# Optimization experiments

Measured on AMD Instinct MI355X. Metric: run time of the kernel, lower is better.

The kernel has to match this reference:

```python
import jax, jax.numpy as jnp
import numpy as np

N_PATHS = 200000
PATH_LEN = 8
N_LINKS = 20000
MAX_PL = 100  # max paths crossing a link
DIM = 16
ITERS = 8
# min-max normalization constants: (min, scale) as in set_min_max_scores
MM_TRAFFIC = (0.0, 1e-4)
MM_PACKETS = (0.0, 1e-2)
MM_PKTSIZE = (0.0, 1e-3)
MM_CAP = (0.0, 1e-1)


def _gru(x, h, k, rk, b):
    # Keras GRUCell, reset_after=True. b: [2, 3*units] (input bias, recurrent bias)
    mx = x @ k + b[0]
    mi = h @ rk + b[1]
    xz, xr, xh = jnp.split(mx, 3, axis=-1)
    rz, rr, rh = jnp.split(mi, 3, axis=-1)
    z = jax.nn.sigmoid(xz + rz)
    r = jax.nn.sigmoid(xr + rr)
    hh = jnp.tanh(xh + r * rh)
    return z * h + (1.0 - z) * hh


def setup_inputs() -> dict:
    key = jax.random.key(0)
    ks = jax.random.split(key, 24)
    f32 = jnp.float32
    inp = {}
    inp['flow_traffic'] = jax.random.uniform(ks[0], (N_PATHS, 1), f32, 100.0, 10000.0)
    inp['flow_packets'] = jax.random.uniform(ks[1], (N_PATHS, 1), f32, 1.0, 100.0)
    inp['flow_packet_size'] = jax.random.uniform(ks[2], (N_PATHS, 1), f32, 100.0, 1500.0)
    inp['flow_type'] = jax.random.uniform(ks[3], (N_PATHS, 2), f32)
    inp['link_capacity'] = jax.random.uniform(ks[4], (N_LINKS, 1), f32, 10.0, 100.0)
    inp['link_to_path'] = jax.random.randint(ks[5], (N_PATHS, PATH_LEN), 0, N_LINKS, jnp.int32)
    p_idx = jax.random.randint(ks[6], (N_LINKS, MAX_PL), 0, N_PATHS, jnp.int32)
    s_idx = jax.random.randint(ks[7], (N_LINKS, MAX_PL), 0, PATH_LEN + 1, jnp.int32)
    inp['path_to_link'] = jnp.stack([p_idx, s_idx], axis=-1)

    def dense(k, i, o):
        return jax.random.normal(k, (i, o), f32) * (1.0 / np.sqrt(i))

    inp['fe_w1'] = dense(ks[8], 5, DIM);   inp['fe_b1'] = jnp.zeros((DIM,), f32)
    inp['fe_w2'] = dense(ks[9], DIM, DIM); inp['fe_b2'] = jnp.zeros((DIM,), f32)
    inp['le_w1'] = dense(ks[10], 2, DIM);  inp['le_b1'] = jnp.zeros((DIM,), f32)
    inp['le_w2'] = dense(ks[11], DIM, DIM); inp['le_b2'] = jnp.zeros((DIM,), f32)
    inp['pgru_k'] = dense(ks[12], DIM, 3 * DIM)
    inp['pgru_rk'] = dense(ks[13], DIM, 3 * DIM)
    inp['pgru_b'] = jnp.zeros((2, 3 * DIM), f32)
    inp['lgru_k'] = dense(ks[14], DIM, 3 * DIM)
    inp['lgru_rk'] = dense(ks[15], DIM, 3 * DIM)
    inp['lgru_b'] = jnp.zeros((2, 3 * DIM), f32)
    inp['ro_w1'] = dense(ks[16], DIM, DIM // 2); inp['ro_b1'] = jnp.zeros((DIM // 2,), f32)
    inp['ro_w2'] = dense(ks[17], DIM // 2, DIM // 4); inp['ro_b2'] = jnp.zeros((DIM // 4,), f32)
    inp['ro_w3'] = dense(ks[18], DIM // 4, 1); inp['ro_b3'] = jnp.zeros((1,), f32)
    return inp


def reference(flow_traffic, flow_packets, flow_packet_size, flow_type, link_capacity,
              link_to_path, path_to_link,
              fe_w1, fe_b1, fe_w2, fe_b2, le_w1, le_b1, le_w2, le_b2,
              pgru_k, pgru_rk, pgru_b, lgru_k, lgru_rk, lgru_b,
              ro_w1, ro_b1, ro_w2, ro_b2, ro_w3, ro_b3):
    relu = jax.nn.relu
    # load per link: sum traffic of crossing paths / capacity
    load = jnp.sum(flow_traffic[path_to_link[:, :, 0]], axis=1) / (link_capacity * 1e9)  # [L,1]

    flow_feats = jnp.concatenate([
        (flow_traffic - MM_TRAFFIC[0]) * MM_TRAFFIC[1],
        (flow_packets - MM_PACKETS[0]) * MM_PACKETS[1],
        (flow_packet_size - MM_PKTSIZE[0]) * MM_PKTSIZE[1],
        flow_type], axis=1)  # [P,5]
    path_state = relu(relu(flow_feats @ fe_w1 + fe_b1) @ fe_w2 + fe_b2)  # [P,16]

    link_feats = jnp.concatenate([(link_capacity - MM_CAP[0]) * MM_CAP[1], load], axis=1)  # [L,2]
    link_state = relu(relu(link_feats @ le_w1 + le_b1) @ le_w2 + le_b2)  # [L,16]

    for _ in range(ITERS):
        link_gather = link_state[link_to_path]  # [P, path_len, 16]
        prev = path_state

        def step(h, x):
            h2 = _gru(x, h, pgru_k, pgru_rk, pgru_b)
            return h2, h2

        path_state, seq = jax.lax.scan(step, prev, jnp.swapaxes(link_gather, 0, 1))
        seq = jnp.swapaxes(seq, 0, 1)  # [P, path_len, 16]
        path_state_sequence = jnp.concatenate([prev[:, None, :], seq], axis=1)  # [P, path_len+1, 16]
        # gather_nd: (path_idx, seq_pos) pairs per link
        path_gather = path_state_sequence[path_to_link[:, :, 0], path_to_link[:, :, 1]]  # [L, MAX_PL, 16]
        path_sum = jnp.sum(path_gather, axis=1)  # [L,16]
        link_state = _gru(path_sum, link_state, lgru_k, lgru_rk, lgru_b)

    h1 = relu(path_state_sequence[:, 1:] @ ro_w1 + ro_b1)
    h2 = relu(h1 @ ro_w2 + ro_b2)
    occupancy = jax.nn.softplus(h2 @ ro_w3 + ro_b3)  # [P, path_len, 1]
    capacity_gather = link_capacity[link_to_path]  # [P, path_len, 1]
    delay = jnp.sum(occupancy / capacity_gather, axis=1)  # [P,1]
    return delay
```

## Files before the change

### kernel.cpp

```cpp
#include <hip/hip_runtime.h>
#include <hip/hip_bf16.h>
#include <math.h>

#define N_PATHS  200000
#define PATH_LEN 8
#define N_LINKS  20000
#define MAX_PL   100
#define DIM      16
#define ITERS    8

typedef __attribute__((ext_vector_type(8))) short bf16x8;
typedef __attribute__((ext_vector_type(4))) float f32x4;

#define SEQ_BYTES 64000000ull
#define LS_BYTES  1280000ull
#define LXK_BYTES 1920000ull
#define P2L_BYTES 8000000ull

__device__ __forceinline__ float fast_sigmoid(float x) {
    return __builtin_amdgcn_rcpf(1.0f + __expf(-x));
}
__device__ __forceinline__ float fast_tanh(float x) {
    float ax = fabsf(x);
    float t  = __expf(-2.0f * ax);
    float r  = (1.0f - t) * __builtin_amdgcn_rcpf(1.0f + t);
    return copysignf(r, x);
}
__device__ __forceinline__ float softplusf_(float x) {
    return fmaxf(x, 0.0f) + log1pf(expf(-fabsf(x)));
}
__device__ __forceinline__ float bflo(unsigned int u) {
    union { unsigned int i; float f; } c; c.i = u << 16; return c.f;
}
__device__ __forceinline__ float bfhi(unsigned int u) {
    union { unsigned int i; float f; } c; c.i = u & 0xffff0000u; return c.f;
}
__device__ __forceinline__ unsigned int pk_bf16(float lo, float hi) {
    unsigned int r;
    asm("v_cvt_pk_bf16_f32 %0, %1, %2" : "=v"(r) : "v"(lo), "v"(hi));
    return r;
}

union U8 { unsigned int u[4]; bf16x8 v; };

__global__ __launch_bounds__(256) void k_pack(const int* __restrict__ p2l,
                                              unsigned int* __restrict__ outE,
                                              unsigned int* __restrict__ outO)
{
    int i = blockIdx.x * 256 + threadIdx.x;
    if (i < N_LINKS * MAX_PL) {
        unsigned int pi = (unsigned int)p2l[2 * i];
        unsigned int si = (unsigned int)p2l[2 * i + 1];
        unsigned int sE = (si == 0) ? 8u : ((si == 8) ? 9u : si);
        unsigned int sO = (si == 0) ? 9u : ((si == 8) ? 8u : si);
        outE[i] = (sE << 18) | pi;
        outO[i] = (sO << 18) | pi;
    }
}

__global__ __launch_bounds__(64) void k_init_links(
    const float* __restrict__ traffic, const float* __restrict__ cap,
    const int* __restrict__ p2l,
    const float* __restrict__ le_w1, const float* __restrict__ le_b1,
    const float* __restrict__ le_w2, const float* __restrict__ le_b2,
    const float* __restrict__ pk, const float* __restrict__ pb,
    float* __restrict__ ls, unsigned short* __restrict__ lxk)
{
    int l = blockIdx.x;
    int lane = threadIdx.x;
    float s = 0.0f;
    for (int j = lane; j < MAX_PL; j += 64) {
        int p = p2l[(size_t)(l * MAX_PL + j) * 2 + 0];
        s += traffic[p];
    }
    #pragma unroll
    for (int off = 32; off > 0; off >>= 1) s += __shfl_xor(s, off);

    float c = cap[l];
    float f0 = c * 0.1f;
    float f1 = s / (c * 1e9f);

    float h1[DIM];
    #pragma unroll
    for (int d = 0; d < DIM; d++)
        h1[d] = fmaxf(f0 * le_w1[d] + f1 * le_w1[DIM + d] + le_b1[d], 0.0f);

    float h2[DIM];
    #pragma unroll
    for (int d = 0; d < DIM; d++) {
        float a = le_b2[d];
        #pragma unroll
        for (int k = 0; k < DIM; k++) a = fmaf(h1[k], le_w2[k * DIM + d], a);
        h2[d] = fmaxf(a, 0.0f);
    }
    if (lane < DIM) ls[(size_t)l * DIM + lane] = h2[lane];
    if (lane < 48) {
        float a = pb[lane];
        #pragma unroll
        for (int k = 0; k < DIM; k++) a = fmaf(h2[k], pk[k * 48 + lane], a);
        lxk[(size_t)l * 48 + lane] = (unsigned short)(pk_bf16(a, a) & 0xffffu);
    }
}

__global__ __launch_bounds__(256) void k_init_paths(
    const float* __restrict__ traffic, const float* __restrict__ packets,
    const float* __restrict__ pktsize, const float* __restrict__ ftype,
    const float* __restrict__ fe_w1, const float* __restrict__ fe_b1,
    const float* __restrict__ fe_w2, const float* __restrict__ fe_b2,
    unsigned short* __restrict__ seq)
{
    int p = blockIdx.x * blockDim.x + threadIdx.x;
    if (p >= N_PATHS) return;
    float f[5];
    f[0] = traffic[p] * 0.0001f;
    f[1] = packets[p] * 0.01f;
    f[2] = pktsize[p] * 0.001f;
    f[3] = ftype[p * 2 + 0];
    f[4] = ftype[p * 2 + 1];

    float h1[DIM];
    #pragma unroll
    for (int d = 0; d < DIM; d++) {
        float a = fe_b1[d];
        #pragma unroll
        for (int k = 0; k < 5; k++) a = fmaf(f[k], fe_w1[k * DIM + d], a);
        h1[d] = fmaxf(a, 0.0f);
    }
    float h2[DIM];
    #pragma unroll
    for (int d = 0; d < DIM; d++) {
        float a = fe_b2[d];
        #pragma unroll
        for (int k = 0; k < DIM; k++) a = fmaf(h1[k], fe_w2[k * DIM + d], a);
        h2[d] = fmaxf(a, 0.0f);
    }
    unsigned int pkd[8];
    #pragma unroll
    for (int q = 0; q < 8; q++) pkd[q] = pk_bf16(h2[2 * q], h2[2 * q + 1]);
    uint4* out = (uint4*)(seq + ((size_t)8 * N_PATHS + p) * DIM);
    out[0] = make_uint4(pkd[0], pkd[1], pkd[2], pkd[3]);
    out[1] = make_uint4(pkd[4], pkd[5], pkd[6], pkd[7]);
}

__global__ __launch_bounds__(256) void k_paths(
    const int* __restrict__ l2p, const unsigned short* __restrict__ lxk,
    const float* __restrict__ rk, const float* __restrict__ b,
    unsigned short* __restrict__ seq, int ps, int cs)
{
    int l = threadIdx.x & 63;
    int wave = (blockIdx.x * 256 + threadIdx.x) >> 6;
    if (wave >= N_PATHS / 32) return;
    int pr = l & 15;
    int g  = l >> 4;
    int kq = g * 4;
    int pA = wave * 32 + pr;
    int pB = pA + 16;

    U8 Az, Ar, Ah;
    {
        #pragma unroll
        for (int i = 0; i < 2; i++) {
            float wz0 = rk[(kq + 2 * i) * 48 + pr] * 0.5f;
            float wz1 = rk[(kq + 2 * i + 1) * 48 + pr] * 0.5f;
            float wr0 = rk[(kq + 2 * i) * 48 + 16 + pr] * 0.5f;
            float wr1 = rk[(kq + 2 * i + 1) * 48 + 16 + pr] * 0.5f;
            float wh0 = rk[(kq + 2 * i) * 48 + 32 + pr] * 0.5f;
            float wh1 = rk[(kq + 2 * i + 1) * 48 + 32 + pr] * 0.5f;
            Az.u[i] = pk_bf16(wz0, wz1); Az.u[i + 2] = Az.u[i];
            Ar.u[i] = pk_bf16(wr0, wr1); Ar.u[i + 2] = Ar.u[i];
            Ah.u[i] = pk_bf16(wh0, wh1); Ah.u[i + 2] = Ah.u[i];
        }
    }
    f32x4 Cz, Cr, Ch;
    #pragma unroll
    for (int r = 0; r < 4; r++) {
        Cz[r] = b[48 + kq + r];
        Cr[r] = b[48 + 16 + kq + r];
        Ch[r] = b[48 + 32 + kq + r];
    }

    int2 iA = *(const int2*)(l2p + (size_t)pA * 8 + 2 * g);
    int2 iB = *(const int2*)(l2p + (size_t)pB * 8 + 2 * g);

    uint2 uzA[8], urA[8], uhA[8];
    uint2 uzB[8], urB[8], uhB[8];

#define PREF(t) { \
    int liA = __shfl(((t) & 1) ? iA.y : iA.x, pr + 16 * ((t) >> 1)); \
    const unsigned short* xa = lxk + (size_t)liA * 48 + kq; \
    uzA[t] = *(const uint2*)(xa); urA[t] = *(const uint2*)(xa + 16); uhA[t] = *(const uint2*)(xa + 32); \
    int liB = __shfl(((t) & 1) ? iB.y : iB.x, pr + 16 * ((t) >> 1)); \
    const unsigned short* xb = lxk + (size_t)liB * 48 + kq; \
    uzB[t] = *(const uint2*)(xb); urB[t] = *(const uint2*)(xb + 16); uhB[t] = *(const uint2*)(xb + 32); }

    PREF(0) PREF(1) PREF(2) PREF(3)

    float hA0, hA1, hA2, hA3, hB0, hB1, hB2, hB3;
    U8 BA, BB;
    {
        uint2 hp = *(const uint2*)(seq + ((size_t)ps * N_PATHS + pA) * DIM + kq);
        hA0 = bflo(hp.x); hA1 = bfhi(hp.x); hA2 = bflo(hp.y); hA3 = bfhi(hp.y);
        BA.u[0] = hp.x; BA.u[1] = hp.y; BA.u[2] = hp.x; BA.u[3] = hp.y;
        uint2 hq = *(const uint2*)(seq + ((size_t)ps * N_PATHS + pB) * DIM + kq);
        hB0 = bflo(hq.x); hB1 = bfhi(hq.x); hB2 = bflo(hq.y); hB3 = bfhi(hq.y);
        BB.u[0] = hq.x; BB.u[1] = hq.y; BB.u[2] = hq.x; BB.u[3] = hq.y;
    }

#define TCORE(t, os, uzX, urX, uhX, BX, h0X, h1X, h2X, h3X, pX) { \
    uint2 uz = uzX[t], ur = urX[t], uh = uhX[t]; \
    f32x4 az = __builtin_amdgcn_mfma_f32_16x16x32_bf16(Az.v, BX.v, Cz, 0, 0, 0); \
    f32x4 ar = __builtin_amdgcn_mfma_f32_16x16x32_bf16(Ar.v, BX.v, Cr, 0, 0, 0); \
    f32x4 ah = __builtin_amdgcn_mfma_f32_16x16x32_bf16(Ah.v, BX.v, Ch, 0, 0, 0); \
    float z0 = fast_sigmoid(bflo(uz.x) + az[0]), z1 = fast_sigmoid(bfhi(uz.x) + az[1]); \
    float z2 = fast_sigmoid(bflo(uz.y) + az[2]), z3 = fast_sigmoid(bfhi(uz.y) + az[3]); \
    float r0 = fast_sigmoid(bflo(ur.x) + ar[0]), r1 = fast_sigmoid(bfhi(ur.x) + ar[1]); \
    float r2 = fast_sigmoid(bflo(ur.y) + ar[2]), r3 = fast_sigmoid(bfhi(ur.y) + ar[3]); \
    float q0 = fast_tanh(bflo(uh.x) + r0 * ah[0]), q1 = fast_tanh(bfhi(uh.x) + r1 * ah[1]); \
    float q2 = fast_tanh(bflo(uh.y) + r2 * ah[2]), q3 = fast_tanh(bfhi(uh.y) + r3 * ah[3]); \
    h0X = z0 * h0X + (1.0f - z0) * q0; \
    h1X = z1 * h1X + (1.0f - z1) * q1; \
    h2X = z2 * h2X + (1.0f - z2) * q2; \
    h3X = z3 * h3X + (1.0f - z3) * q3; \
    unsigned int p01 = pk_bf16(h0X, h1X), p23 = pk_bf16(h2X, h3X); \
    *(uint2*)(seq + ((size_t)(os) * N_PATHS + pX) * DIM + kq) = make_uint2(p01, p23); \
    BX.u[0] = p01; BX.u[1] = p23; BX.u[2] = p01; BX.u[3] = p23; }

#define STEP(t, os) \
    TCORE(t, os, uzA, urA, uhA, BA, hA0, hA1, hA2, hA3, pA) \
    TCORE(t, os, uzB, urB, uhB, BB, hB0, hB1, hB2, hB3, pB)

    PREF(4) STEP(0, 1)
    PREF(5) STEP(1, 2)
    PREF(6) STEP(2, 3)
    PREF(7) STEP(3, 4)
    STEP(4, 5)
    STEP(5, 6)
    STEP(6, 7)
    STEP(7, cs)
#undef PREF
#undef TCORE
#undef STEP
}

__global__ __launch_bounds__(256) void k_links(
    const unsigned int* __restrict__ p2lp, const unsigned short* __restrict__ seq,
    const float* __restrict__ lk, const float* __restrict__ lrk,
    const float* __restrict__ lb,
    const float* __restrict__ pk, const float* __restrict__ pb,
    float* ls, unsigned short* __restrict__ lxk)
{
    int lane = threadIdx.x & 63;
    int l = blockIdx.x * 4 + (threadIdx.x >> 6);
    size_t base = (size_t)l * MAX_PL;
    int half = lane & 1;
    int r0 = lane >> 1;

    unsigned int e0 = p2lp[base + r0];
    unsigned int e1 = p2lp[base + r0 + 32];
    unsigned int e2 = p2lp[base + r0 + 64];

    const unsigned short* sh = seq + half * 8;
    unsigned int pi, si;
    pi = e0 & 0x3FFFFu; si = e0 >> 18;
    uint4 a0 = *(const uint4*)(sh + ((size_t)si * N_PATHS + pi) * DIM);
    pi = e1 & 0x3FFFFu; si = e1 >> 18;
    uint4 a1 = *(const uint4*)(sh + ((size_t)si * N_PATHS + pi) * DIM);
    pi = e2 & 0x3FFFFu; si = e2 >> 18;
    uint4 a2 = *(const uint4*)(sh + ((size_t)si * N_PATHS + pi) * DIM);

    float acc[8];
    #pragma unroll
    for (int i = 0; i < 8; i++) acc[i] = 0.0f;
    unsigned int selLo = 0x00003F80u;
    unsigned int selHi = 0x3F800000u;

#define DOTU(u, i0) \
    asm("v_dot2_f32_bf16 %0, %1, %2, %0" : "+v"(acc[i0]) : "v"(u), "v"(selLo)); \
    asm("v_dot2_f32_bf16 %0, %1, %2, %0" : "+v"(acc[i0 + 1]) : "v"(u), "v"(selHi));
#define DOT8(a) DOTU(a.x, 0) DOTU(a.y, 2) DOTU(a.z, 4) DOTU(a.w, 6)

    DOT8(a0) DOT8(a1) DOT8(a2)
    if (r0 < 4) {
        unsigned int e3 = p2lp[base + r0 + 96];
        pi = e3 & 0x3FFFFu; si = e3 >> 18;
        uint4 a3 = *(const uint4*)(sh + ((size_t)si * N_PATHS + pi) * DIM);
        DOT8(a3)
    }
#undef DOTU
#undef DOT8

    float v4[4];
    {
        int sel = (lane & 2) ? 4 : 0;
        #pragma unroll
        for (int i = 0; i < 4; i++)
            v4[i] = acc[sel + i] + __shfl_xor(acc[(4 - sel) + i], 2);
    }
    float v2[2];
    {
        int sel = (lane & 4) ? 2 : 0;
        #pragma unroll
        for (int i = 0; i < 2; i++)
            v2[i] = v4[sel + i] + __shfl_xor(v4[(2 - sel) + i], 4);
    }
    float s;
    {
        int sel = (lane & 8) ? 1 : 0;
        s = v2[sel] + __shfl_xor(v2[1 - sel], 8);
    }
    s += __shfl_xor(s, 16);
    s += __shfl_xor(s, 32);

    float accf[16];
    #pragma unroll
    for (int k = 0; k < 16; k++) {
        int src = ((k >> 3) & 1) | (((k >> 2) & 1) << 1) | (((k >> 1) & 1) << 2) | ((k & 1) << 3);
        accf[k] = __shfl(s, src);
    }

    float h[DIM];
    #pragma unroll
    for (int d = 0; d < DIM; d++) h[d] = ls[(size_t)l * DIM + d];

    int j = (lane < 48) ? lane : 0;
    float mx = lb[j];
    float mi = lb[48 + j];
    #pragma unroll
    for (int k = 0; k < DIM; k++) {
        mx = fmaf(accf[k], lk[k * 48 + j], mx);
        mi = fmaf(h[k],   lrk[k * 48 + j], mi);
    }

    int d = lane & 15;
    float xz = __shfl(mx, d),      rz = __shfl(mi, d);
    float xr = __shfl(mx, d + 16), rr = __shfl(mi, d + 16);
    float xh = __shfl(mx, d + 32), rh = __shfl(mi, d + 32);
    float z  = fast_sigmoid(xz + rz);
    float r  = fast_sigmoid(xr + rr);
    float hh = fast_tanh(xh + r * rh);
    float hn = z * h[d] + (1.0f - z) * hh;

    if (lane < DIM) ls[(size_t)l * DIM + lane] = hn;

    float hf[DIM];
    #pragma unroll
    for (int k = 0; k < DIM; k++) hf[k] = __shfl(hn, k);
    if (lane < 48) {
        float a = pb[lane];
        #pragma unroll
        for (int k = 0; k < DIM; k++) a = fmaf(hf[k], pk[k * 48 + lane], a);
        lxk[(size_t)l * 48 + lane] = (unsigned short)(pk_bf16(a, a) & 0xffffu);
    }
}

__global__ __launch_bounds__(256) void k_readout(
    const unsigned short* __restrict__ seq, const int* __restrict__ l2p,
    const float* __restrict__ cap,
    const float* __restrict__ w1, const float* __restrict__ b1,
    const float* __restrict__ w2, const float* __restrict__ b2,
    const float* __restrict__ w3, const float* __restrict__ b3,
    float* __restrict__ out)
{
    int p = blockIdx.x * blockDim.x + threadIdx.x;
    if (p >= N_PATHS) return;
    float delay = 0.0f;
    for (int t = 1; t <= PATH_LEN; t++) {
        const uint4* gp = (const uint4*)(seq + ((size_t)t * N_PATHS + p) * DIM);
        uint4 a = gp[0], c = gp[1];
        float h[DIM];
        h[0]  = bflo(a.x); h[1]  = bfhi(a.x); h[2]  = bflo(a.y); h[3]  = bfhi(a.y);
        h[4]  = bflo(a.z); h[5]  = bfhi(a.z); h[6]  = bflo(a.w); h[7]  = bfhi(a.w);
        h[8]  = bflo(c.x); h[9]  = bfhi(c.x); h[10] = bflo(c.y); h[11] = bfhi(c.y);
        h[12] = bflo(c.z); h[13] = bfhi(c.z); h[14] = bflo(c.w); h[15] = bfhi(c.w);

        float h1[8];
        #pragma unroll
        for (int jj = 0; jj < 8; jj++) {
            float a1 = b1[jj];
            #pragma unroll
            for (int k = 0; k < DIM; k++) a1 = fmaf(h[k], w1[k * 8 + jj], a1);
            h1[jj] = fmaxf(a1, 0.0f);
        }
        float h2[4];
        #pragma unroll
        for (int jj = 0; jj < 4; jj++) {
            float a2 = b2[jj];
            #pragma unroll
            for (int k = 0; k < 8; k++) a2 = fmaf(h1[k], w2[k * 4 + jj], a2);
            h2[jj] = fmaxf(a2, 0.0f);
        }
        float o = b3[0];
        #pragma unroll
        for (int k = 0; k < 4; k++) o = fmaf(h2[k], w3[k], o);
        o = softplusf_(o);

        float cp = cap[l2p[(size_t)p * PATH_LEN + (t - 1)]];
        delay += o / cp;
    }
    out[p] = delay;
}

extern "C" void kernel_launch(void* const* d_in, const int* in_sizes, int n_in,
                              void* d_out, int out_size, void* d_ws, size_t ws_size,
                              hipStream_t stream)
{
    const float* flow_traffic = (const float*)d_in[0];
    const float* flow_packets = (const float*)d_in[1];
    const float* flow_pktsize = (const float*)d_in[2];
    const float* flow_type    = (const float*)d_in[3];
    const float* link_cap     = (const float*)d_in[4];
    const int*   l2p          = (const int*)d_in[5];
    const int*   p2l          = (const int*)d_in[6];
    const float* fe_w1 = (const float*)d_in[7];
    const float* fe_b1 = (const float*)d_in[8];
    const float* fe_w2 = (const float*)d_in[9];
    const float* fe_b2 = (const float*)d_in[10];
    const float* le_w1 = (const float*)d_in[11];
    const float* le_b1 = (const float*)d_in[12];
    const float* le_w2 = (const float*)d_in[13];
    const float* le_b2 = (const float*)d_in[14];
    const float* pgru_k  = (const float*)d_in[15];
    const float* pgru_rk = (const float*)d_in[16];
    const float* pgru_b  = (const float*)d_in[17];
    const float* lgru_k  = (const float*)d_in[18];
    const float* lgru_rk = (const float*)d_in[19];
    const float* lgru_b  = (const float*)d_in[20];
    const float* ro_w1 = (const float*)d_in[21];
    const float* ro_b1 = (const float*)d_in[22];
    const float* ro_w2 = (const float*)d_in[23];
    const float* ro_b2 = (const float*)d_in[24];
    const float* ro_w3 = (const float*)d_in[25];
    const float* ro_b3 = (const float*)d_in[26];
    float* out = (float*)d_out;

    char* ws = (char*)d_ws;
    unsigned short* seq   = (unsigned short*)ws;
    float*          ls    = (float*)(ws + SEQ_BYTES);
    unsigned short* lxk   = (unsigned short*)(ws + SEQ_BYTES + LS_BYTES);
    unsigned int*   p2lpE = (unsigned int*)(ws + SEQ_BYTES + LS_BYTES + LXK_BYTES);
    unsigned int*   p2lpO = (unsigned int*)(ws + SEQ_BYTES + LS_BYTES + LXK_BYTES + P2L_BYTES);

    k_pack<<<(N_LINKS * MAX_PL + 255) / 256, 256, 0, stream>>>(p2l, p2lpE, p2lpO);
    k_init_links<<<N_LINKS, 64, 0, stream>>>(flow_traffic, link_cap, p2l,
        le_w1, le_b1, le_w2, le_b2, pgru_k, pgru_b, ls, lxk);
    k_init_paths<<<(N_PATHS + 255) / 256, 256, 0, stream>>>(flow_traffic,
        flow_packets, flow_pktsize, flow_type, fe_w1, fe_b1, fe_w2, fe_b2, seq);

    int nPathBlocks = (N_PATHS / 32 + 3) / 4;
    for (int it = 0; it < ITERS; ++it) {
        int ps = (it & 1) ? 9 : 8;
        int cs = (it & 1) ? 8 : 9;
        k_paths<<<nPathBlocks, 256, 0, stream>>>(l2p, lxk, pgru_rk, pgru_b,
            seq, ps, cs);
        if (it != ITERS - 1)
            k_links<<<N_LINKS / 4, 256, 0, stream>>>((it & 1) ? p2lpO : p2lpE,
                seq, lgru_k, lgru_rk, lgru_b, pgru_k, pgru_b, ls, lxk);
    }

    k_readout<<<(N_PATHS + 255) / 256, 256, 0, stream>>>(seq, l2p, link_cap,
        ro_w1, ro_b1, ro_w2, ro_b2, ro_w3, ro_b3, out);
}
```

Before: 638.3 us.

## Restructure path GRU kernel to one path group per wave with fp32 link projections

The path GRU kernel now gives each wave 16 paths instead of 32, which doubles the number of waves. It drops the interleaved A/B streams and, with launch bounds, asks for four blocks per CU. The precomputed link input projections (lxk) are now stored in fp32 rather than bf16, so the bf16-to-fp32 unpacking goes away at the cost of twice the gather bytes. Gate math is rewritten with packed v_pk_* f32 ops and exp2-based sigmoid and tanh, and address arithmetic uses 32-bit byte offsets. Together these aim to raise occupancy and latency hiding and to cut VALU work, but they add memory traffic on the link gathers.

```diff
diff --git a/kernel.cpp b/kernel.cpp
--- a/kernel.cpp
+++ b/kernel.cpp
@@ -11,11 +11,13 @@
 
 typedef __attribute__((ext_vector_type(8))) short bf16x8;
 typedef __attribute__((ext_vector_type(4))) float f32x4;
+typedef __attribute__((ext_vector_type(2))) float f32x2;
 
 #define SEQ_BYTES 64000000ull
 #define LS_BYTES  1280000ull
-#define LXK_BYTES 1920000ull
+#define LXK_BYTES 3840000ull
 #define P2L_BYTES 8000000ull
+#define SLOT_BYTES 6400000u
 
 __device__ __forceinline__ float fast_sigmoid(float x) {
     return __builtin_amdgcn_rcpf(1.0f + __expf(-x));
@@ -39,6 +41,32 @@
     unsigned int r;
     asm("v_cvt_pk_bf16_f32 %0, %1, %2" : "=v"(r) : "v"(lo), "v"(hi));
     return r;
+}
+
+__device__ __forceinline__ f32x2 pk_add2(f32x2 a, f32x2 b) {
+    f32x2 d; asm("v_pk_add_f32 %0, %1, %2" : "=v"(d) : "v"(a), "v"(b)); return d;
+}
+__device__ __forceinline__ f32x2 pk_mul2(f32x2 a, f32x2 b) {
+    f32x2 d; asm("v_pk_mul_f32 %0, %1, %2" : "=v"(d) : "v"(a), "v"(b)); return d;
+}
+__device__ __forceinline__ f32x2 pk_fma2(f32x2 a, f32x2 b, f32x2 c) {
+    f32x2 d; asm("v_pk_fma_f32 %0, %1, %2, %3" : "=v"(d) : "v"(a), "v"(b), "v"(c)); return d;
+}
+__device__ __forceinline__ f32x2 mk2(float a, float b) { f32x2 r; r.x = a; r.y = b; return r; }
+
+__device__ __forceinline__ f32x2 sig2(f32x2 x) {
+    f32x2 t = pk_mul2(x, mk2(-1.44269504f, -1.44269504f));
+    f32x2 e; e.x = __builtin_amdgcn_exp2f(t.x); e.y = __builtin_amdgcn_exp2f(t.y);
+    f32x2 d = pk_add2(e, mk2(1.0f, 1.0f));
+    f32x2 r; r.x = __builtin_amdgcn_rcpf(d.x); r.y = __builtin_amdgcn_rcpf(d.y);
+    return r;
+}
+__device__ __forceinline__ f32x2 tanh2(f32x2 x) {
+    f32x2 t = pk_mul2(x, mk2(2.88539008f, 2.88539008f));
+    f32x2 e; e.x = __builtin_amdgcn_exp2f(t.x); e.y = __builtin_amdgcn_exp2f(t.y);
+    f32x2 d = pk_add2(e, mk2(1.0f, 1.0f));
+    f32x2 r; r.x = __builtin_amdgcn_rcpf(d.x); r.y = __builtin_amdgcn_rcpf(d.y);
+    return pk_fma2(r, mk2(-2.0f, -2.0f), mk2(1.0f, 1.0f));
 }
 
 union U8 { unsigned int u[4]; bf16x8 v; };
@@ -64,7 +92,7 @@
     const float* __restrict__ le_w1, const float* __restrict__ le_b1,
     const float* __restrict__ le_w2, const float* __restrict__ le_b2,
     const float* __restrict__ pk, const float* __restrict__ pb,
-    float* __restrict__ ls, unsigned short* __restrict__ lxk)
+    float* __restrict__ ls, float* __restrict__ lxk)
 {
     int l = blockIdx.x;
     int lane = threadIdx.x;
@@ -98,7 +126,7 @@
         float a = pb[lane];
         #pragma unroll
         for (int k = 0; k < DIM; k++) a = fmaf(h2[k], pk[k * 48 + lane], a);
-        lxk[(size_t)l * 48 + lane] = (unsigned short)(pk_bf16(a, a) & 0xffffu);
+        lxk[(size_t)l * 48 + lane] = a;
     }
 }
 
@@ -142,19 +170,17 @@
     out[1] = make_uint4(pkd[4], pkd[5], pkd[6], pkd[7]);
 }
 
-__global__ __launch_bounds__(256) void k_paths(
-    const int* __restrict__ l2p, const unsigned short* __restrict__ lxk,
+__global__ __launch_bounds__(256, 4) void k_paths(
+    const int* __restrict__ l2p, const float* __restrict__ lxk,
     const float* __restrict__ rk, const float* __restrict__ b,
     unsigned short* __restrict__ seq, int ps, int cs)
 {
     int l = threadIdx.x & 63;
     int wave = (blockIdx.x * 256 + threadIdx.x) >> 6;
-    if (wave >= N_PATHS / 32) return;
     int pr = l & 15;
     int g  = l >> 4;
     int kq = g * 4;
-    int pA = wave * 32 + pr;
-    int pB = pA + 16;
+    int p  = wave * 16 + pr;
 
     U8 Az, Ar, Ah;
     {
@@ -179,67 +205,66 @@
         Ch[r] = b[48 + 32 + kq + r];
     }
 
-    int2 iA = *(const int2*)(l2p + (size_t)pA * 8 + 2 * g);
-    int2 iB = *(const int2*)(l2p + (size_t)pB * 8 + 2 * g);
-
-    uint2 uzA[8], urA[8], uhA[8];
-    uint2 uzB[8], urB[8], uhB[8];
-
+    int4 ia = *(const int4*)(l2p + (size_t)p * 8);
+    int4 ib = *(const int4*)(l2p + (size_t)p * 8 + 4);
+#define IDX(t) ((t) == 0 ? ia.x : (t) == 1 ? ia.y : (t) == 2 ? ia.z : (t) == 3 ? ia.w : \
+                (t) == 4 ? ib.x : (t) == 5 ? ib.y : (t) == 6 ? ib.z : ib.w)
+
+    const char* lxkc = (const char*)lxk;
+    char* seqc = (char*)seq;
+    unsigned gsh = (unsigned)(g * 16);
+    unsigned sbase = (unsigned)p * 32u + (unsigned)(g * 8);
+    unsigned csoff = (unsigned)cs * SLOT_BYTES + sbase;
+
+    float4 pz[8], prr[8], ph[8];
 #define PREF(t) { \
-    int liA = __shfl(((t) & 1) ? iA.y : iA.x, pr + 16 * ((t) >> 1)); \
-    const unsigned short* xa = lxk + (size_t)liA * 48 + kq; \
-    uzA[t] = *(const uint2*)(xa); urA[t] = *(const uint2*)(xa + 16); uhA[t] = *(const uint2*)(xa + 32); \
-    int liB = __shfl(((t) & 1) ? iB.y : iB.x, pr + 16 * ((t) >> 1)); \
-    const unsigned short* xb = lxk + (size_t)liB * 48 + kq; \
-    uzB[t] = *(const uint2*)(xb); urB[t] = *(const uint2*)(xb + 16); uhB[t] = *(const uint2*)(xb + 32); }
+    unsigned off = (unsigned)IDX(t) * 192u + gsh; \
+    const char* xp = lxkc + off; \
+    pz[t]  = *(const float4*)(xp); \
+    prr[t] = *(const float4*)(xp + 64); \
+    ph[t]  = *(const float4*)(xp + 128); }
 
     PREF(0) PREF(1) PREF(2) PREF(3)
 
-    float hA0, hA1, hA2, hA3, hB0, hB1, hB2, hB3;
-    U8 BA, BB;
+    f32x2 hA, hB;
+    U8 B;
     {
-        uint2 hp = *(const uint2*)(seq + ((size_t)ps * N_PATHS + pA) * DIM + kq);
-        hA0 = bflo(hp.x); hA1 = bfhi(hp.x); hA2 = bflo(hp.y); hA3 = bfhi(hp.y);
-        BA.u[0] = hp.x; BA.u[1] = hp.y; BA.u[2] = hp.x; BA.u[3] = hp.y;
-        uint2 hq = *(const uint2*)(seq + ((size_t)ps * N_PATHS + pB) * DIM + kq);
-        hB0 = bflo(hq.x); hB1 = bfhi(hq.x); hB2 = bflo(hq.y); hB3 = bfhi(hq.y);
-        BB.u[0] = hq.x; BB.u[1] = hq.y; BB.u[2] = hq.x; BB.u[3] = hq.y;
-    }
-
-#define TCORE(t, os, uzX, urX, uhX, BX, h0X, h1X, h2X, h3X, pX) { \
-    uint2 uz = uzX[t], ur = urX[t], uh = uhX[t]; \
-    f32x4 az = __builtin_amdgcn_mfma_f32_16x16x32_bf16(Az.v, BX.v, Cz, 0, 0, 0); \
-    f32x4 ar = __builtin_amdgcn_mfma_f32_16x16x32_bf16(Ar.v, BX.v, Cr, 0, 0, 0); \
-    f32x4 ah = __builtin_amdgcn_mfma_f32_16x16x32_bf16(Ah.v, BX.v, Ch, 0, 0, 0); \
-    float z0 = fast_sigmoid(bflo(uz.x) + az[0]), z1 = fast_sigmoid(bfhi(uz.x) + az[1]); \
-    float z2 = fast_sigmoid(bflo(uz.y) + az[2]), z3 = fast_sigmoid(bfhi(uz.y) + az[3]); \
-    float r0 = fast_sigmoid(bflo(ur.x) + ar[0]), r1 = fast_sigmoid(bfhi(ur.x) + ar[1]); \
-    float r2 = fast_sigmoid(bflo(ur.y) + ar[2]), r3 = fast_sigmoid(bfhi(ur.y) + ar[3]); \
-    float q0 = fast_tanh(bflo(uh.x) + r0 * ah[0]), q1 = fast_tanh(bfhi(uh.x) + r1 * ah[1]); \
-    float q2 = fast_tanh(bflo(uh.y) + r2 * ah[2]), q3 = fast_tanh(bfhi(uh.y) + r3 * ah[3]); \
-    h0X = z0 * h0X + (1.0f - z0) * q0; \
-    h1X = z1 * h1X + (1.0f - z1) * q1; \
-    h2X = z2 * h2X + (1.0f - z2) * q2; \
-    h3X = z3 * h3X + (1.0f - z3) * q3; \
-    unsigned int p01 = pk_bf16(h0X, h1X), p23 = pk_bf16(h2X, h3X); \
-    *(uint2*)(seq + ((size_t)(os) * N_PATHS + pX) * DIM + kq) = make_uint2(p01, p23); \
-    BX.u[0] = p01; BX.u[1] = p23; BX.u[2] = p01; BX.u[3] = p23; }
-
-#define STEP(t, os) \
-    TCORE(t, os, uzA, urA, uhA, BA, hA0, hA1, hA2, hA3, pA) \
-    TCORE(t, os, uzB, urB, uhB, BB, hB0, hB1, hB2, hB3, pB)
-
-    PREF(4) STEP(0, 1)
-    PREF(5) STEP(1, 2)
-    PREF(6) STEP(2, 3)
-    PREF(7) STEP(3, 4)
-    STEP(4, 5)
-    STEP(5, 6)
-    STEP(6, 7)
-    STEP(7, cs)
+        uint2 hp = *(const uint2*)(seqc + ((unsigned)ps * SLOT_BYTES + sbase));
+        hA = mk2(bflo(hp.x), bfhi(hp.x));
+        hB = mk2(bflo(hp.y), bfhi(hp.y));
+        B.u[0] = hp.x; B.u[1] = hp.y; B.u[2] = hp.x; B.u[3] = hp.y;
+    }
+
+#define STEPX(t, soff) { \
+    f32x4 az = __builtin_amdgcn_mfma_f32_16x16x32_bf16(Az.v, B.v, Cz, 0, 0, 0); \
+    f32x4 ar = __builtin_amdgcn_mfma_f32_16x16x32_bf16(Ar.v, B.v, Cr, 0, 0, 0); \
+    f32x4 ah = __builtin_amdgcn_mfma_f32_16x16x32_bf16(Ah.v, B.v, Ch, 0, 0, 0); \
+    f32x2 zA = sig2(pk_add2(mk2(pz[t].x, pz[t].y), mk2(az[0], az[1]))); \
+    f32x2 zB = sig2(pk_add2(mk2(pz[t].z, pz[t].w), mk2(az[2], az[3]))); \
+    f32x2 rA = sig2(pk_add2(mk2(prr[t].x, prr[t].y), mk2(ar[0], ar[1]))); \
+    f32x2 rB = sig2(pk_add2(mk2(prr[t].z, prr[t].w), mk2(ar[2], ar[3]))); \
+    f32x2 qA = tanh2(pk_fma2(rA, mk2(ah[0], ah[1]), mk2(ph[t].x, ph[t].y))); \
+    f32x2 qB = tanh2(pk_fma2(rB, mk2(ah[2], ah[3]), mk2(ph[t].z, ph[t].w))); \
+    f32x2 dA = pk_fma2(qA, mk2(-1.0f, -1.0f), hA); \
+    f32x2 dB = pk_fma2(qB, mk2(-1.0f, -1.0f), hB); \
+    hA = pk_fma2(zA, dA, qA); \
+    hB = pk_fma2(zB, dB, qB); \
+    unsigned int p01 = pk_bf16(hA.x, hA.y); \
+    unsigned int p23 = pk_bf16(hB.x, hB.y); \
+    *(uint2*)(seqc + (soff)) = make_uint2(p01, p23); \
+    B.u[0] = p01; B.u[1] = p23; B.u[2] = p01; B.u[3] = p23; }
+
+    STEPX(0, 1u * SLOT_BYTES + sbase)  PREF(4)
+    STEPX(1, 2u * SLOT_BYTES + sbase)  PREF(5)
+    STEPX(2, 3u * SLOT_BYTES + sbase)  PREF(6)
+    STEPX(3, 4u * SLOT_BYTES + sbase)  PREF(7)
+    STEPX(4, 5u * SLOT_BYTES + sbase)
+    STEPX(5, 6u * SLOT_BYTES + sbase)
+    STEPX(6, 7u * SLOT_BYTES + sbase)
+    STEPX(7, csoff)
 #undef PREF
-#undef TCORE
-#undef STEP
+#undef STEPX
+#undef IDX
 }
 
 __global__ __launch_bounds__(256) void k_links(
@@ -247,7 +272,7 @@
     const float* __restrict__ lk, const float* __restrict__ lrk,
     const float* __restrict__ lb,
     const float* __restrict__ pk, const float* __restrict__ pb,
-    float* ls, unsigned short* __restrict__ lxk)
+    float* ls, float* __restrict__ lxk)
 {
     int lane = threadIdx.x & 63;
     int l = blockIdx.x * 4 + (threadIdx.x >> 6);
@@ -349,7 +374,7 @@
         float a = pb[lane];
         #pragma unroll
         for (int k = 0; k < DIM; k++) a = fmaf(hf[k], pk[k * 48 + lane], a);
-        lxk[(size_t)l * 48 + lane] = (unsigned short)(pk_bf16(a, a) & 0xffffu);
+        lxk[(size_t)l * 48 + lane] = a;
     }
 }
 
@@ -436,7 +461,7 @@
     char* ws = (char*)d_ws;
     unsigned short* seq   = (unsigned short*)ws;
     float*          ls    = (float*)(ws + SEQ_BYTES);
-    unsigned short* lxk   = (unsigned short*)(ws + SEQ_BYTES + LS_BYTES);
+    float*          lxk   = (float*)(ws + SEQ_BYTES + LS_BYTES);
     unsigned int*   p2lpE = (unsigned int*)(ws + SEQ_BYTES + LS_BYTES + LXK_BYTES);
     unsigned int*   p2lpO = (unsigned int*)(ws + SEQ_BYTES + LS_BYTES + LXK_BYTES + P2L_BYTES);
 
@@ -446,12 +471,11 @@
     k_init_paths<<<(N_PATHS + 255) / 256, 256, 0, stream>>>(flow_traffic,
         flow_packets, flow_pktsize, flow_type, fe_w1, fe_b1, fe_w2, fe_b2, seq);
 
-    int nPathBlocks = (N_PATHS / 32 + 3) / 4;
     for (int it = 0; it < ITERS; ++it) {
         int ps = (it & 1) ? 9 : 8;
         int cs = (it & 1) ? 8 : 9;
-        k_paths<<<nPathBlocks, 256, 0, stream>>>(l2p, lxk, pgru_rk, pgru_b,
-            seq, ps, cs);
+        k_paths<<<(N_PATHS / 16) / 4, 256, 0, stream>>>(l2p, lxk, pgru_rk,
+            pgru_b, seq, ps, cs);
         if (it != ITERS - 1)
             k_links<<<N_LINKS / 4, 256, 0, stream>>>((it & 1) ? p2lpO : p2lpE,
                 seq, lgru_k, lgru_rk, lgru_b, pgru_k, pgru_b, ls, lxk);
```

After: 637.6 us. About the same (-0.1%).
